# Optimization experiments

Measured on AMD Instinct MI355X. Metric: run time of the kernel, lower is better.

## Reference

```python
import jax, jax.numpy as jnp
import numpy as np

V, H, L = 32000, 512, 1
B, S = 16, 64


def setup_inputs() -> dict:
    key = jax.random.key(0)
    ks = jax.random.split(key, 10)
    inp = {
        "target_seqs": jax.random.randint(ks[0], (B, S), 0, V),
        "thought": jax.random.normal(ks[1], (1, B, H), dtype=jnp.float32),
        "hidden": jax.random.normal(ks[2], (L, B, H), dtype=jnp.float32),
        # parameters
        "emb": jax.random.normal(ks[3], (V, H), dtype=jnp.float32) * 0.02,
        "W_ih": jax.random.normal(ks[4], (3 * H, 2 * H), dtype=jnp.float32) * (1.0 / np.sqrt(H)),
        "W_hh": jax.random.normal(ks[5], (3 * H, H), dtype=jnp.float32) * (1.0 / np.sqrt(H)),
        "b_ih": jax.random.normal(ks[6], (3 * H,), dtype=jnp.float32) * 0.01,
        "b_hh": jax.random.normal(ks[7], (3 * H,), dtype=jnp.float32) * 0.01,
        "W_out": jax.random.normal(ks[8], (V, H), dtype=jnp.float32) * (1.0 / np.sqrt(H)),
        "b_out": jax.random.normal(ks[9], (V,), dtype=jnp.float32) * 0.01,
    }
    return inp


def gru_layer(x_sbd, h0, W_ih, W_hh, b_ih, b_hh):
    # x_sbd: [S,B,2H]; h0: [B,H]. Torch GRU cell math.
    # Precompute input projections for all timesteps: [S,B,3H]
    gi = jnp.einsum('sbd,gd->sbg', x_sbd, W_ih) + b_ih

    def step(h, gi_t):
        gh = h @ W_hh.T + b_hh                       # [B,3H]
        i_r, i_z, i_n = jnp.split(gi_t, 3, axis=-1)
        h_r, h_z, h_n = jnp.split(gh, 3, axis=-1)
        r = jax.nn.sigmoid(i_r + h_r)
        z = jax.nn.sigmoid(i_z + h_z)
        n = jnp.tanh(i_n + r * h_n)
        h_new = (1.0 - z) * n + z * h
        return h_new, h_new

    h_last, ys = jax.lax.scan(step, h0, gi)
    return ys, h_last                                 # [S,B,H], [B,H]


def reference(target_seqs, thought, hidden, emb, W_ih, W_hh, b_ih, b_hh, W_out, b_out):
    embedded = emb[target_seqs]                        # [B,S,H]
    # fused broadcast-concat replacing the python double loop
    th = jnp.broadcast_to(thought[0][:, None, :], embedded.shape)  # [B,S,H]
    rnn_input = jnp.concatenate([embedded, th], axis=-1)           # [B,S,2H]
    x_sbd = jnp.transpose(rnn_input, (1, 0, 2))                    # [S,B,2H]
    ys, h_last = gru_layer(x_sbd, hidden[0], W_ih, W_hh, b_ih, b_hh)
    output = jnp.transpose(ys, (1, 0, 2))              # [B,S,H]
    logits = jnp.einsum('bsh,vh->bsv', output, W_out) + b_out
    logp = jax.nn.log_softmax(logits, axis=-1)         # [B,S,V]
    return logp, h_last[None]                          # hidden: [1,B,H]
```

## Files before the change

kernel.cpp:

```cpp
#include <hip/hip_runtime.h>

typedef unsigned int u32;
typedef unsigned short u16;
typedef short s16x8 __attribute__((ext_vector_type(8)));
typedef float f32x4 __attribute__((ext_vector_type(4)));

#define SENT 0xFFFFFFFFu

__device__ __forceinline__ u16 f2bf(float f) {
  u32 u = __float_as_uint(f);
  u32 r = (u + 0x7fffu + ((u >> 16) & 1u)) >> 16;
  return (u16)r;
}

__device__ __forceinline__ uint4 load_u4_bypass(const u32* p) {
  uint4 r;
  asm volatile("global_load_dwordx4 %0, %1, off sc0 sc1\n\ts_waitcnt vmcnt(0)"
               : "=v"(r) : "v"(p) : "memory");
  return r;
}

__global__ __launch_bounds__(256) void cvt_bf16_kernel(const float* __restrict__ src,
                                                       u16* __restrict__ dst, int n4) {
  int i = blockIdx.x * 256 + threadIdx.x;
  if (i >= n4) return;
  float4 v = reinterpret_cast<const float4*>(src)[i];
  u32 lo = (u32)f2bf(v.x) | ((u32)f2bf(v.y) << 16);
  u32 hi = (u32)f2bf(v.z) | ((u32)f2bf(v.w) << 16);
  reinterpret_cast<uint2*>(dst)[i] = make_uint2(lo, hi);
}

__global__ __launch_bounds__(128) void build_x_kernel(const int* __restrict__ tseq,
                                                      const float* __restrict__ emb,
                                                      const float* __restrict__ thought,
                                                      u16* __restrict__ x) {
  int m = blockIdx.x;
  int s = m >> 4, b = m & 15;
  int tid = threadIdx.x;
  int k = tid * 8;
  const float* src;
  if (k < 512) src = emb + (size_t)tseq[b * 64 + s] * 512 + k;
  else         src = thought + b * 512 + (k - 512);
  float4 v0 = reinterpret_cast<const float4*>(src)[0];
  float4 v1 = reinterpret_cast<const float4*>(src)[1];
  uint4 o;
  o.x = (u32)f2bf(v0.x) | ((u32)f2bf(v0.y) << 16);
  o.y = (u32)f2bf(v0.z) | ((u32)f2bf(v0.w) << 16);
  o.z = (u32)f2bf(v1.x) | ((u32)f2bf(v1.y) << 16);
  o.w = (u32)f2bf(v1.z) | ((u32)f2bf(v1.w) << 16);
  *reinterpret_cast<uint4*>(x + (size_t)m * 1024 + k) = o;
}

template <bool LSE>
__global__ __launch_bounds__(256) void gemm_bt_kernel(const u16* __restrict__ A,
                                                      const u16* __restrict__ Bm,
                                                      const float* __restrict__ bias,
                                                      float* __restrict__ C,
                                                      int M_, int N_, int K_,
                                                      float* __restrict__ partials, int nnb) {
  __shared__ u16 sA[128 * 40];
  __shared__ u16 sB[128 * 40];
  __shared__ float pm[2][128];
  __shared__ float ps[2][128];
  int nb = blockIdx.x, mb = blockIdx.y;
  int m0 = mb * 128, n0 = nb * 128;
  int tid = threadIdx.x;
  int wave = tid >> 6, lane = tid & 63;
  int wm = wave >> 1, wn = wave & 1;
  int l16 = lane & 15, quad = lane >> 4;
  int srow = tid >> 1, shalf = tid & 1;
  const u16* gA = A + (size_t)(m0 + srow) * K_ + shalf * 16;
  const u16* gB = Bm + (size_t)(n0 + srow) * K_ + shalf * 16;
  u16* lA = &sA[srow * 40 + shalf * 16];
  u16* lB = &sB[srow * 40 + shalf * 16];
  f32x4 acc[4][4];
  for (int i = 0; i < 4; ++i)
    for (int j = 0; j < 4; ++j) acc[i][j] = (f32x4){0.f, 0.f, 0.f, 0.f};

  for (int k0 = 0; k0 < K_; k0 += 32) {
    uint4 a0 = *reinterpret_cast<const uint4*>(gA + k0);
    uint4 a1 = *reinterpret_cast<const uint4*>(gA + k0 + 8);
    uint4 b0 = *reinterpret_cast<const uint4*>(gB + k0);
    uint4 b1 = *reinterpret_cast<const uint4*>(gB + k0 + 8);
    __syncthreads();
    *reinterpret_cast<uint4*>(lA) = a0;
    *reinterpret_cast<uint4*>(lA + 8) = a1;
    *reinterpret_cast<uint4*>(lB) = b0;
    *reinterpret_cast<uint4*>(lB + 8) = b1;
    __syncthreads();
    s16x8 af[4], bfr[4];
    for (int mt = 0; mt < 4; ++mt)
      af[mt] = *reinterpret_cast<const s16x8*>(&sA[(wm * 64 + mt * 16 + l16) * 40 + quad * 8]);
    for (int nt = 0; nt < 4; ++nt)
      bfr[nt] = *reinterpret_cast<const s16x8*>(&sB[(wn * 64 + nt * 16 + l16) * 40 + quad * 8]);
    for (int mt = 0; mt < 4; ++mt)
      for (int nt = 0; nt < 4; ++nt)
        acc[mt][nt] = __builtin_amdgcn_mfma_f32_16x16x32_bf16(af[mt], bfr[nt], acc[mt][nt], 0, 0, 0);
  }

  int rbase = wm * 64 + quad * 4;
  int cbase = n0 + wn * 64 + l16;
  for (int nt = 0; nt < 4; ++nt) {
    float bv = bias[cbase + nt * 16];
    for (int mt = 0; mt < 4; ++mt)
      for (int r = 0; r < 4; ++r) acc[mt][nt][r] += bv;
  }
  for (int mt = 0; mt < 4; ++mt)
    for (int r = 0; r < 4; ++r) {
      int row = m0 + rbase + mt * 16 + r;
      for (int nt = 0; nt < 4; ++nt)
        C[(size_t)row * N_ + cbase + nt * 16] = acc[mt][nt][r];
    }
  if (LSE) {
    for (int mt = 0; mt < 4; ++mt)
      for (int r = 0; r < 4; ++r) {
        float mx = acc[mt][0][r];
        for (int nt = 1; nt < 4; ++nt) mx = fmaxf(mx, acc[mt][nt][r]);
        for (int d = 1; d < 16; d <<= 1) mx = fmaxf(mx, __shfl_xor(mx, d));
        float sm = 0.f;
        for (int nt = 0; nt < 4; ++nt) sm += __expf(acc[mt][nt][r] - mx);
        for (int d = 1; d < 16; d <<= 1) sm += __shfl_xor(sm, d);
        if (l16 == 0) {
          int rr = wm * 64 + mt * 16 + quad * 4 + r;
          pm[wn][rr] = mx;
          ps[wn][rr] = sm;
        }
      }
    __syncthreads();
    if (tid < 128) {
      float m1 = pm[0][tid], m2 = pm[1][tid];
      float s1 = ps[0][tid], s2 = ps[1][tid];
      float Mx = fmaxf(m1, m2);
      float Sx = s1 * __expf(m1 - Mx) + s2 * __expf(m2 - Mx);
      float* p = partials + ((size_t)(m0 + tid) * nnb + nb) * 2;
      p[0] = Mx;
      p[1] = Sx;
    }
  }
}

__global__ __launch_bounds__(256, 2) void gru_kernel(const float* __restrict__ gi,
                                                     const float* __restrict__ W_hh,
                                                     const float* __restrict__ b_hh,
                                                     const float* __restrict__ hidden,
                                                     u32* __restrict__ hbase,
                                                     u16* __restrict__ ys,
                                                     float* __restrict__ hlast,
                                                     const float* __restrict__ wout_f32,
                                                     u16* __restrict__ wout_bf) {
  __shared__ u16 sW[48 * 520];
  __shared__ float h_s[576];
  int wg = blockIdx.x;
  int tid = threadIdx.x;

  if (wg >= 512) {
    for (int i = (wg - 512) * 256 + tid; i < 4096000; i += 256 * 256) {
      float4 v = reinterpret_cast<const float4*>(wout_f32)[i];
      u32 lo = (u32)f2bf(v.x) | ((u32)f2bf(v.y) << 16);
      u32 hi = (u32)f2bf(v.z) | ((u32)f2bf(v.w) << 16);
      reinterpret_cast<uint2*>(wout_bf)[i] = make_uint2(lo, hi);
    }
    return;
  }

  int b = wg >> 5, g = wg & 31;
  for (int e = tid * 4; e < 48 * 512; e += 1024) {
    int lr = e >> 9, col = e & 511;
    int grow = (lr >> 4) * 512 + g * 16 + (lr & 15);
    float4 v = *reinterpret_cast<const float4*>(W_hh + (size_t)grow * 512 + col);
    u32 lo = (u32)f2bf(v.x) | ((u32)f2bf(v.y) << 16);
    u32 hi = (u32)f2bf(v.z) | ((u32)f2bf(v.w) << 16);
    *reinterpret_cast<uint2*>(&sW[lr * 520 + col]) = make_uint2(lo, hi);
  }
  int grp = tid >> 4, l16 = tid & 15;
  int j = g * 16 + grp;
  float bhr = 0.f, bhz = 0.f, bhn = 0.f;
  if (l16 == 0) { bhr = b_hh[j]; bhz = b_hh[512 + j]; bhn = b_hh[1024 + j]; }
  int j0 = tid * 4;
  if (tid < 128) {
    float4 f = *reinterpret_cast<const float4*>(hidden + b * 512 + j0);
    *reinterpret_cast<float4*>(&h_s[j0 + ((j0 >> 5) << 2)]) = f;
  }
  __syncthreads();

  for (int t = 0; t < 64; ++t) {
    float gir = 0.f, giz = 0.f, gin = 0.f;
    if (l16 == 0) {
      size_t gib = ((size_t)t * 16 + b) * 1536;
      gir = gi[gib + j]; giz = gi[gib + 512 + j]; gin = gi[gib + 1024 + j];
    }
    if (t > 0) {
      const u32* hp = hbase + (size_t)(t - 1) * 8192 + b * 512;
      if (tid < 32) {
        const u32* fp = hp + tid * 16;
        u32 v = __hip_atomic_load(fp, __ATOMIC_RELAXED, __HIP_MEMORY_SCOPE_AGENT);
        while (v == SENT) {
          __builtin_amdgcn_s_sleep(2);
          v = __hip_atomic_load(fp, __ATOMIC_RELAXED, __HIP_MEMORY_SCOPE_AGENT);
        }
      }
      __syncthreads();
      if (tid < 128) {
        uint4 v = load_u4_bypass(hp + j0);
        while (v.x == SENT || v.y == SENT || v.z == SENT || v.w == SENT) {
          __builtin_amdgcn_s_sleep(1);
          v = load_u4_bypass(hp + j0);
        }
        float4 f;
        f.x = __uint_as_float(v.x); f.y = __uint_as_float(v.y);
        f.z = __uint_as_float(v.z); f.w = __uint_as_float(v.w);
        *reinterpret_cast<float4*>(&h_s[j0 + ((j0 >> 5) << 2)]) = f;
      }
      __syncthreads();
    }
    float hreg[32];
    int hb2 = l16 * 36;
    for (int c4 = 0; c4 < 4; ++c4) {
      float4 x0 = *reinterpret_cast<const float4*>(&h_s[hb2 + c4 * 8]);
      float4 x1 = *reinterpret_cast<const float4*>(&h_s[hb2 + c4 * 8 + 4]);
      hreg[c4 * 8 + 0] = x0.x; hreg[c4 * 8 + 1] = x0.y;
      hreg[c4 * 8 + 2] = x0.z; hreg[c4 * 8 + 3] = x0.w;
      hreg[c4 * 8 + 4] = x1.x; hreg[c4 * 8 + 5] = x1.y;
      hreg[c4 * 8 + 6] = x1.z; hreg[c4 * 8 + 7] = x1.w;
    }
    float a0 = 0.f, a1 = 0.f, a2 = 0.f;
    const u16* wr0 = &sW[grp * 520 + l16 * 32];
    const u16* wr1 = wr0 + 16 * 520;
    const u16* wr2 = wr0 + 32 * 520;
    for (int c4 = 0; c4 < 4; ++c4) {
      uint4 w0 = *reinterpret_cast<const uint4*>(wr0 + c4 * 8);
      uint4 w1 = *reinterpret_cast<const uint4*>(wr1 + c4 * 8);
      uint4 w2 = *reinterpret_cast<const uint4*>(wr2 + c4 * 8);
      const float* hh = &hreg[c4 * 8];
      a0 += __uint_as_float(w0.x << 16) * hh[0] + __uint_as_float(w0.x & 0xffff0000u) * hh[1];
      a0 += __uint_as_float(w0.y << 16) * hh[2] + __uint_as_float(w0.y & 0xffff0000u) * hh[3];
      a0 += __uint_as_float(w0.z << 16) * hh[4] + __uint_as_float(w0.z & 0xffff0000u) * hh[5];
      a0 += __uint_as_float(w0.w << 16) * hh[6] + __uint_as_float(w0.w & 0xffff0000u) * hh[7];
      a1 += __uint_as_float(w1.x << 16) * hh[0] + __uint_as_float(w1.x & 0xffff0000u) * hh[1];
      a1 += __uint_as_float(w1.y << 16) * hh[2] + __uint_as_float(w1.y & 0xffff0000u) * hh[3];
      a1 += __uint_as_float(w1.z << 16) * hh[4] + __uint_as_float(w1.z & 0xffff0000u) * hh[5];
      a1 += __uint_as_float(w1.w << 16) * hh[6] + __uint_as_float(w1.w & 0xffff0000u) * hh[7];
      a2 += __uint_as_float(w2.x << 16) * hh[0] + __uint_as_float(w2.x & 0xffff0000u) * hh[1];
      a2 += __uint_as_float(w2.y << 16) * hh[2] + __uint_as_float(w2.y & 0xffff0000u) * hh[3];
      a2 += __uint_as_float(w2.z << 16) * hh[4] + __uint_as_float(w2.z & 0xffff0000u) * hh[5];
      a2 += __uint_as_float(w2.w << 16) * hh[6] + __uint_as_float(w2.w & 0xffff0000u) * hh[7];
    }
    for (int d = 1; d < 16; d <<= 1) {
      a0 += __shfl_xor(a0, d);
      a1 += __shfl_xor(a1, d);
      a2 += __shfl_xor(a2, d);
    }
    if (l16 == 0) {
      float er = __expf(-(gir + a0 + bhr));
      float ez = __expf(-(giz + a1 + bhz));
      float r = __fdividef(1.f, 1.f + er);
      float z = __fdividef(1.f, 1.f + ez);
      float xn = gin + r * (a2 + bhn);
      float en = __expf(2.f * xn);
      float n = 1.f - __fdividef(2.f, en + 1.f);
      float hprev = h_s[j + ((j >> 5) << 2)];
      float hv = (1.f - z) * n + z * hprev;
      __hip_atomic_store(hbase + (size_t)t * 8192 + b * 512 + j, __float_as_uint(hv),
                         __ATOMIC_RELAXED, __HIP_MEMORY_SCOPE_AGENT);
      ys[((size_t)b * 64 + t) * 512 + j] = f2bf(hv);
      if (t == 63) hlast[b * 512 + j] = hv;
    }
  }
}

__global__ __launch_bounds__(64) void lse_combine_kernel(const float* __restrict__ partials,
                                                         float* __restrict__ lse, int nnb) {
  int row = blockIdx.x;
  int lane = threadIdx.x;
  float M = -INFINITY, S = 0.f;
  for (int i = lane; i < nnb; i += 64) {
    const float* p = partials + ((size_t)row * nnb + i) * 2;
    float m2 = p[0], s2 = p[1];
    if (m2 > M) { float tt = M; M = m2; m2 = tt; tt = S; S = s2; s2 = tt; }
    if (s2 > 0.f) S += s2 * __expf(m2 - M);
  }
  for (int d = 1; d < 64; d <<= 1) {
    float m2 = __shfl_xor(M, d), s2 = __shfl_xor(S, d);
    if (m2 > M) { float tt = M; M = m2; m2 = tt; tt = S; S = s2; s2 = tt; }
    if (s2 > 0.f) S += s2 * __expf(m2 - M);
  }
  if (lane == 0) lse[row] = M + logf(S);
}

__global__ __launch_bounds__(256) void sub_lse_kernel(float* __restrict__ out,
                                                      const float* __restrict__ lse) {
  int i = blockIdx.x * 256 + threadIdx.x;
  int row = i / 8000;
  float l = lse[row];
  float4 v = reinterpret_cast<float4*>(out)[i];
  v.x -= l; v.y -= l; v.z -= l; v.w -= l;
  reinterpret_cast<float4*>(out)[i] = v;
}

extern "C" void kernel_launch(void* const* d_in, const int* in_sizes, int n_in,
                              void* d_out, int out_size, void* d_ws, size_t ws_size,
                              hipStream_t stream) {
  const int* tseq = (const int*)d_in[0];
  const float* thought = (const float*)d_in[1];
  const float* hidden = (const float*)d_in[2];
  const float* emb = (const float*)d_in[3];
  const float* W_ih = (const float*)d_in[4];
  const float* W_hh = (const float*)d_in[5];
  const float* b_ih = (const float*)d_in[6];
  const float* b_hh = (const float*)d_in[7];
  const float* W_out = (const float*)d_in[8];
  const float* b_out = (const float*)d_in[9];
  float* out = (float*)d_out;

  char* ws = (char*)d_ws;
  size_t off = 0;
  auto alloc = [&](size_t bytes) {
    void* p = ws + off;
    off = (off + bytes + 255) & ~(size_t)255;
    return p;
  };
  u16* wout_bf = (u16*)alloc((size_t)32000 * 512 * 2);
  u16* wih_bf  = (u16*)alloc((size_t)1536 * 1024 * 2);
  u16* x_bf    = (u16*)alloc((size_t)1024 * 1024 * 2);
  u16* ys_bf   = (u16*)alloc((size_t)1024 * 512 * 2);
  float* gi    = (float*)alloc((size_t)1024 * 1536 * 4);
  u32* hbase   = (u32*)alloc((size_t)64 * 16 * 512 * 4);
  float* partials = (float*)alloc((size_t)1024 * 250 * 2 * 4);
  float* lse   = (float*)alloc((size_t)1024 * 4);
  (void)ws_size; (void)in_sizes; (void)n_in; (void)out_size;

  hipMemsetAsync(hbase, 0xFF, (size_t)64 * 16 * 512 * 4, stream);
  cvt_bf16_kernel<<<1536, 256, 0, stream>>>(W_ih, wih_bf, 393216);
  build_x_kernel<<<1024, 128, 0, stream>>>(tseq, emb, thought, x_bf);
  gemm_bt_kernel<false><<<dim3(12, 8), 256, 0, stream>>>(x_bf, wih_bf, b_ih, gi,
                                                         1024, 1536, 1024, nullptr, 0);
  gru_kernel<<<768, 256, 0, stream>>>(gi, W_hh, b_hh, hidden, hbase, ys_bf,
                                      out + 32768000, W_out, wout_bf);
  gemm_bt_kernel<true><<<dim3(250, 8), 256, 0, stream>>>(ys_bf, wout_bf, b_out, out,
                                                         1024, 32000, 512, partials, 250);
  lse_combine_kernel<<<1024, 64, 0, stream>>>(partials, lse, 250);
  sub_lse_kernel<<<32000, 256, 0, stream>>>(out, lse);
}
```

Baseline: 484.4 us.

## Double-buffer GEMM tiles with direct global-to-LDS loads

The bf16 GEMM main loop now copies A and B tiles straight from global memory into shared memory with `global_load_lds`, into two alternating buffers. The next K-slice is fetched while MFMAs run on the current one, which removes the register round-trip and one of the two barriers per iteration. In exchange the shared-memory row stride drops from a padded 40 to an unpadded 32 elements, which may add bank conflicts on fragment reads. Correctness also depends on the barrier waiting for the asynchronous LDS loads to finish.

Measured after the change: 473.2 us. -2.3%, faster.

```diff
diff --git a/kernel.cpp b/kernel.cpp
--- a/kernel.cpp
+++ b/kernel.cpp
@@ -18,6 +18,12 @@
   asm volatile("global_load_dwordx4 %0, %1, off sc0 sc1\n\ts_waitcnt vmcnt(0)"
                : "=v"(r) : "v"(p) : "memory");
   return r;
+}
+
+__device__ __forceinline__ void gload16(const u16* g, u16* l) {
+  __builtin_amdgcn_global_load_lds(
+      (const __attribute__((address_space(1))) unsigned int*)(g),
+      (__attribute__((address_space(3))) unsigned int*)(l), 16, 0, 0);
 }
 
 __global__ __launch_bounds__(256) void cvt_bf16_kernel(const float* __restrict__ src,
@@ -58,8 +64,8 @@
                                                       float* __restrict__ C,
                                                       int M_, int N_, int K_,
                                                       float* __restrict__ partials, int nnb) {
-  __shared__ u16 sA[128 * 40];
-  __shared__ u16 sB[128 * 40];
+  __shared__ u16 sA[2][4096];
+  __shared__ u16 sB[2][4096];
   __shared__ float pm[2][128];
   __shared__ float ps[2][128];
   int nb = blockIdx.x, mb = blockIdx.y;
@@ -68,34 +74,44 @@
   int wave = tid >> 6, lane = tid & 63;
   int wm = wave >> 1, wn = wave & 1;
   int l16 = lane & 15, quad = lane >> 4;
-  int srow = tid >> 1, shalf = tid & 1;
-  const u16* gA = A + (size_t)(m0 + srow) * K_ + shalf * 16;
-  const u16* gB = Bm + (size_t)(n0 + srow) * K_ + shalf * 16;
-  u16* lA = &sA[srow * 40 + shalf * 16];
-  u16* lB = &sB[srow * 40 + shalf * 16];
+  int c0 = wave * 128 + lane, c1 = c0 + 64;
+  int r0 = c0 >> 2, co0 = (c0 & 3) * 8;
+  int r1 = c1 >> 2, co1 = (c1 & 3) * 8;
+  const u16* gA0 = A + (size_t)(m0 + r0) * K_ + co0;
+  const u16* gA1 = A + (size_t)(m0 + r1) * K_ + co1;
+  const u16* gB0 = Bm + (size_t)(n0 + r0) * K_ + co0;
+  const u16* gB1 = Bm + (size_t)(n0 + r1) * K_ + co1;
+  int wbase = wave * 1024;
+
+  auto STAGE = [&](int buf, int k0) {
+    gload16(gA0 + k0, &sA[buf][wbase]);
+    gload16(gA1 + k0, &sA[buf][wbase + 512]);
+    gload16(gB0 + k0, &sB[buf][wbase]);
+    gload16(gB1 + k0, &sB[buf][wbase + 512]);
+  };
+
   f32x4 acc[4][4];
   for (int i = 0; i < 4; ++i)
     for (int j = 0; j < 4; ++j) acc[i][j] = (f32x4){0.f, 0.f, 0.f, 0.f};
 
-  for (int k0 = 0; k0 < K_; k0 += 32) {
-    uint4 a0 = *reinterpret_cast<const uint4*>(gA + k0);
-    uint4 a1 = *reinterpret_cast<const uint4*>(gA + k0 + 8);
-    uint4 b0 = *reinterpret_cast<const uint4*>(gB + k0);
-    uint4 b1 = *reinterpret_cast<const uint4*>(gB + k0 + 8);
-    __syncthreads();
-    *reinterpret_cast<uint4*>(lA) = a0;
-    *reinterpret_cast<uint4*>(lA + 8) = a1;
-    *reinterpret_cast<uint4*>(lB) = b0;
-    *reinterpret_cast<uint4*>(lB + 8) = b1;
-    __syncthreads();
+  int NK = K_ >> 5;
+  STAGE(0, 0);
+  __syncthreads();
+  int cur = 0;
+  for (int ks = 0; ks < NK; ++ks) {
+    if (ks + 1 < NK) STAGE(cur ^ 1, (ks + 1) * 32);
     s16x8 af[4], bfr[4];
     for (int mt = 0; mt < 4; ++mt)
-      af[mt] = *reinterpret_cast<const s16x8*>(&sA[(wm * 64 + mt * 16 + l16) * 40 + quad * 8]);
+      af[mt] = *reinterpret_cast<const s16x8*>(&sA[cur][(wm * 64 + mt * 16 + l16) * 32 + quad * 8]);
     for (int nt = 0; nt < 4; ++nt)
-      bfr[nt] = *reinterpret_cast<const s16x8*>(&sB[(wn * 64 + nt * 16 + l16) * 40 + quad * 8]);
+      bfr[nt] = *reinterpret_cast<const s16x8*>(&sB[cur][(wn * 64 + nt * 16 + l16) * 32 + quad * 8]);
     for (int mt = 0; mt < 4; ++mt)
       for (int nt = 0; nt < 4; ++nt)
         acc[mt][nt] = __builtin_amdgcn_mfma_f32_16x16x32_bf16(af[mt], bfr[nt], acc[mt][nt], 0, 0, 0);
+    if (ks + 1 < NK) {
+      __syncthreads();
+      cur ^= 1;
+    }
   }
 
   int rbase = wm * 64 + quad * 4;
```
